# Kernel tuning notes

Hardware: AMD Instinct MI355X
Metric: run time of the kernel (lower is better)

## Reference

```python
import jax, jax.numpy as jnp
import numpy as np

P = 1  # scoring_norm (L1 distance, no GEMM shortcut)

def _lp_norm(v, p):
    # torch.norm(v, p=p, dim=-1)
    if p == 1:
        return jnp.sum(jnp.abs(v), axis=-1)
    return jnp.sum(jnp.abs(v) ** p, axis=-1) ** (1.0 / p)

def setup_inputs() -> dict:
    key = jax.random.key(0)
    k1, k2, k3, k4 = jax.random.split(key, 4)
    batch, n_neg, d, n_rel = 512, 2048, 128, 1000
    return {
        "head_emb": jax.random.normal(k1, (batch, d), dtype=jnp.float32),
        "relation_id": jax.random.randint(k2, (batch,), 0, n_rel, dtype=jnp.int64),
        "tail_emb": jax.random.normal(k3, (1, n_neg, d), dtype=jnp.float32),
        "relation_embedding": jax.random.normal(k4, (n_rel, d), dtype=jnp.float32),
    }

def reference(head_emb, relation_id, tail_emb, relation_embedding):
    # TransE.score_tails with negative_sample_sharing=True
    d = head_emb.shape[-1]
    rel = relation_embedding[relation_id]            # (batch, d)
    v1 = head_emb + rel                              # (batch, d) query
    v2 = tail_emb.reshape(-1, d)                     # (B*n_neg, d)
    diff = v1[:, None, :] - v2[None, :, :]           # (batch, B*n_neg, d)
    return -_lp_norm(diff, P)                        # (batch, B*n_neg)
```

## Files before the change

### kernel.cpp

```cpp
#include <hip/hip_runtime.h>

#define BATCH 512
#define NNEG  2048
#define DIM   128


__global__ __launch_bounds__(256, 2)
void transe_l1(const float* __restrict__ head,
               const int*   __restrict__ relid,
               const float* __restrict__ tailp,
               const float* __restrict__ relemb,
               float* __restrict__ out) {
  __shared__ float lds[96 * 128];
  float* lt = lds;
  float* lq = lds + 64 * 128;

  const int tid = threadIdx.x;
  const int bx  = blockIdx.x;
  const int t0  = (bx & 31) * 64;
  const int b0  = (bx >> 5) * 32;

#pragma unroll
  for (int m = 0; m < 8; ++m) {
    int k = tid + m * 256;
    int r = k >> 5, g = k & 31;
    float4 v = *reinterpret_cast<const float4*>(&tailp[(t0 + r) * DIM + g * 4]);
    int p = g ^ (r & 7);
    *reinterpret_cast<float4*>(&lt[r * 128 + p * 4]) = v;
  }
#pragma unroll
  for (int m = 0; m < 4; ++m) {
    int k = tid + m * 256;
    int r = k >> 5, g = k & 31;
    int b = b0 + r;
    int rid = relid[b];
    float4 h = *reinterpret_cast<const float4*>(&head[b * DIM + g * 4]);
    float4 e = *reinterpret_cast<const float4*>(&relemb[rid * DIM + g * 4]);
    float4 v;
    v.x = h.x + e.x; v.y = h.y + e.y; v.z = h.z + e.z; v.w = h.w + e.w;
    int p = (g >> 2) + (g & 3) * 8;
    *reinterpret_cast<float4*>(&lq[r * 128 + p * 4]) = v;
  }
  __syncthreads();

  const int lane = tid & 63;
  const int w    = tid >> 6;
  const int tg   = lane & 7;
  const int dg   = lane >> 3;

  float4 tf[8][4];
#pragma unroll
  for (int k = 0; k < 8; ++k) {
#pragma unroll
    for (int j = 0; j < 4; ++j) {
      int p = (dg * 4 + j) ^ tg;
      tf[k][j] = *reinterpret_cast<const float4*>(&lt[(8 * k + tg) * 128 + p * 4]);
    }
  }

  float acc[8][8];
#pragma unroll
  for (int r = 0; r < 8; ++r)
#pragma unroll
    for (int k = 0; k < 8; ++k) acc[r][k] = 0.f;

  const int qbase = (w * 8) * 128;
#pragma unroll
  for (int r = 0; r < 8; ++r) {
    float4 qf[4];
#pragma unroll
    for (int j = 0; j < 4; ++j)
      qf[j] = *reinterpret_cast<const float4*>(&lq[qbase + r * 128 + (dg + 8 * j) * 4]);
#pragma unroll
    for (int k = 0; k < 8; ++k) {
#pragma unroll
      for (int j = 0; j < 4; ++j) {
        acc[r][k] += fabsf(qf[j].x - tf[k][j].x);
        acc[r][k] += fabsf(qf[j].y - tf[k][j].y);
        acc[r][k] += fabsf(qf[j].z - tf[k][j].z);
        acc[r][k] += fabsf(qf[j].w - tf[k][j].w);
      }
    }
  }

  const int brow = b0 + w * 8 + dg;
#pragma unroll
  for (int k = 0; k < 8; ++k) {
    float s4[4];
#pragma unroll
    for (int i = 0; i < 4; ++i) {
      float a  = acc[2 * i][k], b = acc[2 * i + 1][k];
      float xa = __shfl_xor(a, 8), xb = __shfl_xor(b, 8);
      s4[i] = (dg & 1) ? (b + xb) : (a + xa);
    }
    float s2[2];
#pragma unroll
    for (int i = 0; i < 2; ++i) {
      float a  = s4[2 * i], b = s4[2 * i + 1];
      float xa = __shfl_xor(a, 16), xb = __shfl_xor(b, 16);
      s2[i] = (dg & 2) ? (b + xb) : (a + xa);
    }
    float a  = s2[0], b = s2[1];
    float xa = __shfl_xor(a, 32), xb = __shfl_xor(b, 32);
    float v  = (dg & 4) ? (b + xb) : (a + xa);
    out[brow * NNEG + t0 + 8 * k + tg] = -v;
  }
}

extern "C" void kernel_launch(void* const* d_in, const int* in_sizes, int n_in,
                              void* d_out, int out_size, void* d_ws, size_t ws_size,
                              hipStream_t stream) {
  const float* head   = (const float*)d_in[0];
  const int*   relid  = (const int*)d_in[1];
  const float* tailp  = (const float*)d_in[2];
  const float* relemb = (const float*)d_in[3];
  float*       out    = (float*)d_out;

  transe_l1<<<dim3(512), dim3(256), 0, stream>>>(head, relid, tailp, relemb, out);
}
```

Baseline: 15.05 us.

## Load tail tiles directly to registers and split reduction into two halves

Tail embeddings are now loaded straight from global memory into registers, in two halves across the dimension, so the tail LDS staging buffer is gone and the register footprint for tail fragments is halved. The query tile in LDS uses padded rows instead of an XOR swizzle. The xor-8 and xor-16 cross-lane reductions use ds_swizzle instead of generic shuffles. The aim is less LDS traffic and lower register pressure. The cost is a second global load phase in the middle of the compute loop, which may expose latency, and a possibly different LDS bank-conflict pattern for the query reads.

Result: slower. 18.00 us (+19.7%).

```diff
diff --git a/kernel.cpp b/kernel.cpp
--- a/kernel.cpp
+++ b/kernel.cpp
@@ -3,7 +3,15 @@
 #define BATCH 512
 #define NNEG  2048
 #define DIM   128
+#define PADR  132
 
+
+__device__ __forceinline__ float swz8(float v) {
+  return __int_as_float(__builtin_amdgcn_ds_swizzle(__float_as_int(v), 0x201F));
+}
+__device__ __forceinline__ float swz16(float v) {
+  return __int_as_float(__builtin_amdgcn_ds_swizzle(__float_as_int(v), 0x401F));
+}
 
 __global__ __launch_bounds__(256, 2)
 void transe_l1(const float* __restrict__ head,
@@ -11,23 +19,26 @@
                const float* __restrict__ tailp,
                const float* __restrict__ relemb,
                float* __restrict__ out) {
-  __shared__ float lds[96 * 128];
-  float* lt = lds;
-  float* lq = lds + 64 * 128;
+  __shared__ float lq[32 * PADR];
 
-  const int tid = threadIdx.x;
-  const int bx  = blockIdx.x;
-  const int t0  = (bx & 31) * 64;
-  const int b0  = (bx >> 5) * 32;
+  const int tid  = threadIdx.x;
+  const int bx   = blockIdx.x;
+  const int t0   = (bx & 31) * 64;
+  const int b0   = (bx >> 5) * 32;
+  const int lane = tid & 63;
+  const int w    = tid >> 6;
+  const int tg   = lane & 7;
+  const int dg   = lane >> 3;
 
+  const float* tbase = tailp + (size_t)(t0 + tg) * DIM + 4 * dg;
+  float4 tf[8][2];
 #pragma unroll
-  for (int m = 0; m < 8; ++m) {
-    int k = tid + m * 256;
-    int r = k >> 5, g = k & 31;
-    float4 v = *reinterpret_cast<const float4*>(&tailp[(t0 + r) * DIM + g * 4]);
-    int p = g ^ (r & 7);
-    *reinterpret_cast<float4*>(&lt[r * 128 + p * 4]) = v;
+  for (int k = 0; k < 8; ++k) {
+#pragma unroll
+    for (int j = 0; j < 2; ++j)
+      tf[k][j] = *reinterpret_cast<const float4*>(tbase + (size_t)(8 * k) * DIM + 32 * j);
   }
+
 #pragma unroll
   for (int m = 0; m < 4; ++m) {
     int k = tid + m * 256;
@@ -38,25 +49,9 @@
     float4 e = *reinterpret_cast<const float4*>(&relemb[rid * DIM + g * 4]);
     float4 v;
     v.x = h.x + e.x; v.y = h.y + e.y; v.z = h.z + e.z; v.w = h.w + e.w;
-    int p = (g >> 2) + (g & 3) * 8;
-    *reinterpret_cast<float4*>(&lq[r * 128 + p * 4]) = v;
+    *reinterpret_cast<float4*>(&lq[r * PADR + g * 4]) = v;
   }
   __syncthreads();
-
-  const int lane = tid & 63;
-  const int w    = tid >> 6;
-  const int tg   = lane & 7;
-  const int dg   = lane >> 3;
-
-  float4 tf[8][4];
-#pragma unroll
-  for (int k = 0; k < 8; ++k) {
-#pragma unroll
-    for (int j = 0; j < 4; ++j) {
-      int p = (dg * 4 + j) ^ tg;
-      tf[k][j] = *reinterpret_cast<const float4*>(&lt[(8 * k + tg) * 128 + p * 4]);
-    }
-  }
 
   float acc[8][8];
 #pragma unroll
@@ -64,21 +59,34 @@
 #pragma unroll
     for (int k = 0; k < 8; ++k) acc[r][k] = 0.f;
 
-  const int qbase = (w * 8) * 128;
+  const float* lqw = lq + (w * 8) * PADR;
+
 #pragma unroll
-  for (int r = 0; r < 8; ++r) {
-    float4 qf[4];
+  for (int p = 0; p < 2; ++p) {
+    if (p == 1) {
 #pragma unroll
-    for (int j = 0; j < 4; ++j)
-      qf[j] = *reinterpret_cast<const float4*>(&lq[qbase + r * 128 + (dg + 8 * j) * 4]);
+      for (int k = 0; k < 8; ++k) {
 #pragma unroll
-    for (int k = 0; k < 8; ++k) {
+        for (int j = 0; j < 2; ++j)
+          tf[k][j] = *reinterpret_cast<const float4*>(tbase + (size_t)(8 * k) * DIM + 32 * (2 + j));
+      }
+    }
 #pragma unroll
-      for (int j = 0; j < 4; ++j) {
-        acc[r][k] += fabsf(qf[j].x - tf[k][j].x);
-        acc[r][k] += fabsf(qf[j].y - tf[k][j].y);
-        acc[r][k] += fabsf(qf[j].z - tf[k][j].z);
-        acc[r][k] += fabsf(qf[j].w - tf[k][j].w);
+    for (int r = 0; r < 8; ++r) {
+      float4 q0 = *reinterpret_cast<const float4*>(&lqw[r * PADR + (8 * (2 * p + 0) + dg) * 4]);
+      float4 q1 = *reinterpret_cast<const float4*>(&lqw[r * PADR + (8 * (2 * p + 1) + dg) * 4]);
+#pragma unroll
+      for (int k = 0; k < 8; ++k) {
+        float s = acc[r][k];
+        s += fabsf(q0.x - tf[k][0].x);
+        s += fabsf(q0.y - tf[k][0].y);
+        s += fabsf(q0.z - tf[k][0].z);
+        s += fabsf(q0.w - tf[k][0].w);
+        s += fabsf(q1.x - tf[k][1].x);
+        s += fabsf(q1.y - tf[k][1].y);
+        s += fabsf(q1.z - tf[k][1].z);
+        s += fabsf(q1.w - tf[k][1].w);
+        acc[r][k] = s;
       }
     }
   }
@@ -90,20 +98,20 @@
 #pragma unroll
     for (int i = 0; i < 4; ++i) {
       float a  = acc[2 * i][k], b = acc[2 * i + 1][k];
-      float xa = __shfl_xor(a, 8), xb = __shfl_xor(b, 8);
+      float xa = swz8(a), xb = swz8(b);
       s4[i] = (dg & 1) ? (b + xb) : (a + xa);
     }
     float s2[2];
 #pragma unroll
     for (int i = 0; i < 2; ++i) {
       float a  = s4[2 * i], b = s4[2 * i + 1];
-      float xa = __shfl_xor(a, 16), xb = __shfl_xor(b, 16);
+      float xa = swz16(a), xb = swz16(b);
       s2[i] = (dg & 2) ? (b + xb) : (a + xa);
     }
     float a  = s2[0], b = s2[1];
     float xa = __shfl_xor(a, 32), xb = __shfl_xor(b, 32);
     float v  = (dg & 4) ? (b + xb) : (a + xa);
-    out[brow * NNEG + t0 + 8 * k + tg] = -v;
+    out[(size_t)brow * NNEG + t0 + 8 * k + tg] = -v;
   }
 }
 
```
